# Optimization experiments

Measured on AMD Instinct MI355X. Metric: run time of the kernel, lower is better.

The kernel has to match this reference:

```python
import jax, jax.numpy as jnp
import numpy as np

N, E, DIM, H = 50000, 800000, 64, 2
HD = H * DIM


def setup_inputs() -> dict:
    key = jax.random.key(0)
    ks = jax.random.split(key, 16)
    s = 0.05
    return {
        "x": jax.random.normal(ks[0], (N, DIM), jnp.float32),
        "edge_index": jax.random.randint(ks[1], (2, E), 0, N, jnp.int64),
        "Wq": jax.random.normal(ks[2], (DIM, HD), jnp.float32) * s,
        "bq": jax.random.normal(ks[3], (HD,), jnp.float32) * s,
        "Wk": jax.random.normal(ks[4], (DIM, HD), jnp.float32) * s,
        "bk": jax.random.normal(ks[5], (HD,), jnp.float32) * s,
        "Wv": jax.random.normal(ks[6], (DIM, HD), jnp.float32) * s,
        "bv": jax.random.normal(ks[7], (HD,), jnp.float32) * s,
        "Wskip": jax.random.normal(ks[8], (DIM, HD), jnp.float32) * s,
        "bskip": jax.random.normal(ks[9], (HD,), jnp.float32) * s,
        "Wc": jax.random.normal(ks[10], (HD, DIM), jnp.float32) * s,
        "bc": jax.random.normal(ks[11], (DIM,), jnp.float32) * s,
        "gamma": jnp.ones((DIM,), jnp.float32),
        "beta": jnp.zeros((DIM,), jnp.float32),
    }


def reference(x, edge_index, Wq, bq, Wk, bk, Wv, bv, Wskip, bskip, Wc, bc, gamma, beta):
    src, dst = edge_index[0], edge_index[1]  # messages flow src -> dst
    # TransformerConv: per-head q/k/v projections, [N, H, D]
    q = (x @ Wq + bq).reshape(N, H, DIM)
    k = (x @ Wk + bk).reshape(N, H, DIM)
    v = (x @ Wv + bv).reshape(N, H, DIM)
    scale = 1.0 / np.sqrt(DIM).astype(np.float32)
    # edge-wise attention logits: [E, H]
    alpha = jnp.einsum('ehd,ehd->eh', q[dst], k[src]) * scale
    # segment softmax over incoming edges of each dst node (PyG softmax)
    amax = jax.ops.segment_max(alpha, dst, num_segments=N)
    a = jnp.exp(alpha - amax[dst])
    asum = jax.ops.segment_sum(a, dst, num_segments=N)
    a = a / (asum[dst] + 1e-16)
    # weighted scatter-aggregate of values: [N, H, D] -> concat heads
    out = jax.ops.segment_sum(a[:, :, None] * v[src], dst, num_segments=N)
    out = out.reshape(N, HD)
    # root/skip connection (root_weight=True default)
    out = out + (x @ Wskip + bskip)
    # concat linear: H*D -> dim
    out = out @ Wc + bc
    # pyg.LayerNorm default mode='graph': normalize over ALL nodes+features
    out = out - out.mean()
    out = out / (out.std() + 1e-5)  # std with unbiased=False (jnp default ddof=0)
    return out * gamma + beta
```

## Files before the change

### kernel.cpp

```cpp
#include <hip/hip_runtime.h>
#include <hip/hip_bf16.h>

#define N_NODES 50000
#define N_EDGES 800000
#define DIM 64
#define NHEAD 2
#define HD 128
#define NCOL 448
#define MAXDEG 64

#define ACH 2048
#define EDGE_BLKS 391

#define PREP_B 112
#define PROJ_B 782

#define QSCALE 0.18033688011112042f

typedef short bf16x8 __attribute__((ext_vector_type(8)));
typedef float f32x16 __attribute__((ext_vector_type(16)));
typedef float f32x2 __attribute__((ext_vector_type(2)));

__device__ __forceinline__ unsigned short f2bf(float f) {
    unsigned u = __float_as_uint(f);
    unsigned r = (u + 0x7fffu + ((u >> 16) & 1u)) >> 16;
    return (unsigned short)r;
}
__device__ __forceinline__ unsigned char f2fp8(float f) {
    int r = __builtin_amdgcn_cvt_pk_fp8_f32(f, f, 0, false);
    return (unsigned char)(r & 0xff);
}

__global__ __launch_bounds__(256) void k_pb(
    const int* __restrict__ ei,
    const float* __restrict__ Wq, const float* __restrict__ bq,
    const float* __restrict__ Wk, const float* __restrict__ bk,
    const float* __restrict__ Wv, const float* __restrict__ bv,
    const float* __restrict__ Wskip, const float* __restrict__ bskip,
    const float* __restrict__ Wc, const float* __restrict__ bc,
    unsigned short* __restrict__ WallT, float* __restrict__ ball,
    int* __restrict__ deg, unsigned short* __restrict__ elist,
    double* __restrict__ stats)
{
    const int t = threadIdx.x;
    if (blockIdx.x < PREP_B) {
        int gid = blockIdx.x * 256 + t;
        if (gid == 0) { stats[0] = 0.0; stats[1] = 0.0; }
        const int j = gid >> 6;
        const int d = gid & 63;
        float w, bb;
        if (j < 128) {
            w = Wq[d * HD + j] * QSCALE;
            bb = bq[j] * QSCALE;
        } else if (j < 256) {
            int jj = j - 128;
            w = Wk[d * HD + jj];
            bb = bk[jj];
        } else if (j < 384) {
            int jj = j - 256;
            int h = jj >> 6, jc = jj & 63;
            float s = 0.f, sb = 0.f;
            for (int c = 0; c < 64; c++) {
                float wc = Wc[(h * 64 + c) * DIM + jc];
                s  += Wv[d * HD + h * 64 + c] * wc;
                sb += bv[h * 64 + c] * wc;
            }
            w = s; bb = sb;
        } else {
            int jj = j - 384;
            float s = 0.f, sb = bc[jj];
            for (int c = 0; c < HD; c++) {
                float wc = Wc[c * DIM + jj];
                s  += Wskip[d * HD + c] * wc;
                sb += bskip[c] * wc;
            }
            w = s; bb = sb;
        }
        WallT[gid] = f2bf(w);
        if (d == 0) ball[j] = bb;
        return;
    }
    const int e0 = (blockIdx.x - PREP_B) * ACH;
#pragma unroll 2
    for (int i = t; i < ACH; i += 256) {
        int e = e0 + i;
        if (e < N_EDGES) {
            int src = ei[e];
            int d = ei[N_EDGES + e];
            int sl = atomicAdd(&deg[d], 1);
            if (sl < MAXDEG)
                elist[(size_t)d * MAXDEG + sl] = (unsigned short)src;
        }
    }
}

__global__ __launch_bounds__(256) void k_ep(
    const float* __restrict__ x,
    const unsigned short* __restrict__ WallT, const float* __restrict__ ball,
    float* __restrict__ q, unsigned char* __restrict__ kv, float* __restrict__ skipc)
{
    const int blk = blockIdx.x;
    const int t = threadIdx.x;
    const int w = t >> 6;
    const int lane = t & 63;
    const int col = lane & 31;
    const int khalf = lane >> 5;
    const int n0 = blk * 64 + (w >> 1) * 32;
    const int ct0 = (w & 1) * 7;
    const int rowbase = 4 * khalf;

    int nread = n0 + col; if (nread >= N_NODES) nread = N_NODES - 1;
    const float* ap = x + (size_t)nread * 64 + khalf * 8;
    bf16x8 afrag[4];
#pragma unroll
    for (int kk = 0; kk < 4; kk++) {
        float4 xa = *((const float4*)(ap + kk * 16));
        float4 xb4 = *((const float4*)(ap + kk * 16 + 4));
        bf16x8 f;
        f[0] = (short)f2bf(xa.x); f[1] = (short)f2bf(xa.y);
        f[2] = (short)f2bf(xa.z); f[3] = (short)f2bf(xa.w);
        f[4] = (short)f2bf(xb4.x); f[5] = (short)f2bf(xb4.y);
        f[6] = (short)f2bf(xb4.z); f[7] = (short)f2bf(xb4.w);
        afrag[kk] = f;
    }

    for (int tt = 0; tt < 7; tt++) {
        const int gc = (ct0 + tt) * 32 + col;
        const float b = ball[gc];
        f32x16 acc;
#pragma unroll
        for (int r = 0; r < 16; r++) acc[r] = b;
        const unsigned short* bp = WallT + (size_t)gc * 64 + khalf * 8;
#pragma unroll
        for (int kk = 0; kk < 4; kk++) {
            bf16x8 bfrag = *((const bf16x8*)(bp + kk * 16));
            acc = __builtin_amdgcn_mfma_f32_32x32x16_bf16(afrag[kk], bfrag, acc, 0, 0, 0);
        }
        if (gc < 128) {
#pragma unroll
            for (int r = 0; r < 16; r++) {
                int node = n0 + (r & 3) + 8 * (r >> 2) + rowbase;
                if (node < N_NODES) q[(size_t)node * HD + gc] = acc[r];
            }
        } else if (gc < 384) {
            int ch = gc - 128;
            int half = ch >> 7;
            int cc = ch & 127;
            int h = cc >> 6, c = cc & 63;
            int pos = half * 128 + ((c >> 3) << 4) + (h << 3) + (c & 7);
#pragma unroll
            for (int r = 0; r < 16; r++) {
                int node = n0 + (r & 3) + 8 * (r >> 2) + rowbase;
                if (node < N_NODES) kv[(size_t)node * 256 + pos] = f2fp8(acc[r]);
            }
        } else {
#pragma unroll
            for (int r = 0; r < 16; r++) {
                int node = n0 + (r & 3) + 8 * (r >> 2) + rowbase;
                if (node < N_NODES) skipc[(size_t)node * DIM + (gc - 384)] = acc[r];
            }
        }
    }
}

__global__ __launch_bounds__(256) void k_attn(
    const float* __restrict__ q, const unsigned char* __restrict__ kv,
    const float* __restrict__ skipc,
    const int* __restrict__ deg, const unsigned short* __restrict__ elist,
    float* __restrict__ out, float* __restrict__ parts)
{
    const int w = threadIdx.x >> 6;
    const int lane = threadIdx.x & 63;
    const int g = lane >> 3;
    const int j = lane & 7;
    const int n = blockIdx.x * 4 + w;
    const f32x2* qp = (const f32x2*)(q + (size_t)n * HD);
    f32x2 q0[4], q1[4];
#pragma unroll
    for (int i = 0; i < 4; i++) { q0[i] = qp[4 * j + i]; q1[i] = qp[32 + 4 * j + i]; }
    const int myE = elist[(size_t)n * MAXDEG + lane];
    f32x2 acc0[4], acc1[4];
#pragma unroll
    for (int i = 0; i < 4; i++) {
        acc0[i] = (f32x2){0.f, 0.f};
        acc1[i] = (f32x2){0.f, 0.f};
    }
    float l0 = 0.f, l1 = 0.f;
    int dg = deg[n]; if (dg > MAXDEG) dg = MAXDEG;
    for (int b0 = 0; b0 < dg; b0 += 8) {
        int idx = b0 + g;
        bool valid = idx < dg;
        int s = __shfl(myE, valid ? idx : 0, 64);
        const uint4* kp = (const uint4*)(kv + (size_t)s * 256);
        uint4 K = kp[j];
        uint4 V = kp[8 + j];
        f32x2 p0v = q0[0] * __builtin_amdgcn_cvt_pk_f32_fp8(K.x, false);
        p0v += q0[1] * __builtin_amdgcn_cvt_pk_f32_fp8(K.x, true);
        p0v += q0[2] * __builtin_amdgcn_cvt_pk_f32_fp8(K.y, false);
        p0v += q0[3] * __builtin_amdgcn_cvt_pk_f32_fp8(K.y, true);
        f32x2 p1v = q1[0] * __builtin_amdgcn_cvt_pk_f32_fp8(K.z, false);
        p1v += q1[1] * __builtin_amdgcn_cvt_pk_f32_fp8(K.z, true);
        p1v += q1[2] * __builtin_amdgcn_cvt_pk_f32_fp8(K.w, false);
        p1v += q1[3] * __builtin_amdgcn_cvt_pk_f32_fp8(K.w, true);
        float p0 = p0v[0] + p0v[1];
        float p1 = p1v[0] + p1v[1];
#pragma unroll
        for (int off = 1; off < 8; off <<= 1) {
            p0 += __shfl_xor(p0, off, 64);
            p1 += __shfl_xor(p1, off, 64);
        }
        float w0 = valid ? __builtin_amdgcn_exp2f(p0) : 0.f;
        float w1 = valid ? __builtin_amdgcn_exp2f(p1) : 0.f;
        l0 += w0; l1 += w1;
        f32x2 w0v = {w0, w0}, w1v = {w1, w1};
        acc0[0] += w0v * __builtin_amdgcn_cvt_pk_f32_fp8(V.x, false);
        acc0[1] += w0v * __builtin_amdgcn_cvt_pk_f32_fp8(V.x, true);
        acc0[2] += w0v * __builtin_amdgcn_cvt_pk_f32_fp8(V.y, false);
        acc0[3] += w0v * __builtin_amdgcn_cvt_pk_f32_fp8(V.y, true);
        acc1[0] += w1v * __builtin_amdgcn_cvt_pk_f32_fp8(V.z, false);
        acc1[1] += w1v * __builtin_amdgcn_cvt_pk_f32_fp8(V.z, true);
        acc1[2] += w1v * __builtin_amdgcn_cvt_pk_f32_fp8(V.w, false);
        acc1[3] += w1v * __builtin_amdgcn_cvt_pk_f32_fp8(V.w, true);
    }
    float* a0 = (float*)acc0;
    float* a1 = (float*)acc1;
#pragma unroll
    for (int off = 8; off < 64; off <<= 1) {
        l0 += __shfl_xor(l0, off, 64);
        l1 += __shfl_xor(l1, off, 64);
#pragma unroll
        for (int i = 0; i < 8; i++) {
            a0[i] += __shfl_xor(a0[i], off, 64);
            a1[i] += __shfl_xor(a1[i], off, 64);
        }
    }
    if (g == 0) {
        float inv0 = 1.f / (l0 + 1e-16f), inv1 = 1.f / (l1 + 1e-16f);
        const float4* sk = (const float4*)(skipc + (size_t)n * DIM);
        float4 sa = sk[2 * j], sb = sk[2 * j + 1];
        float o[8];
        o[0] = a0[0] * inv0 + a1[0] * inv1 + sa.x;
        o[1] = a0[1] * inv0 + a1[1] * inv1 + sa.y;
        o[2] = a0[2] * inv0 + a1[2] * inv1 + sa.z;
        o[3] = a0[3] * inv0 + a1[3] * inv1 + sa.w;
        o[4] = a0[4] * inv0 + a1[4] * inv1 + sb.x;
        o[5] = a0[5] * inv0 + a1[5] * inv1 + sb.y;
        o[6] = a0[6] * inv0 + a1[6] * inv1 + sb.z;
        o[7] = a0[7] * inv0 + a1[7] * inv1 + sb.w;
        float4 r0 = {o[0], o[1], o[2], o[3]}, r1 = {o[4], o[5], o[6], o[7]};
        float4* op = (float4*)(out + (size_t)n * DIM);
        op[2 * j] = r0; op[2 * j + 1] = r1;
        float s_ = 0.f, ss = 0.f;
#pragma unroll
        for (int i = 0; i < 8; i++) { s_ += o[i]; ss += o[i] * o[i]; }
#pragma unroll
        for (int off = 1; off < 8; off <<= 1) {
            s_ += __shfl_xor(s_, off, 64);
            ss += __shfl_xor(ss, off, 64);
        }
        if (j == 0) { parts[n] = s_; parts[N_NODES + n] = ss; }
    }
}

#define RED_BLOCKS 100
__global__ __launch_bounds__(256) void k_reduce(
    const float* __restrict__ parts, double* __restrict__ stats)
{
    double s = 0.0, ss = 0.0;
    for (int i = blockIdx.x * 256 + threadIdx.x; i < N_NODES; i += RED_BLOCKS * 256) {
        s  += (double)parts[i];
        ss += (double)parts[N_NODES + i];
    }
#pragma unroll
    for (int off = 32; off > 0; off >>= 1) {
        s  += __shfl_down(s, off);
        ss += __shfl_down(ss, off);
    }
    __shared__ double sdd[8];
    int wave = threadIdx.x >> 6;
    if ((threadIdx.x & 63) == 0) { sdd[wave * 2] = s; sdd[wave * 2 + 1] = ss; }
    __syncthreads();
    if (threadIdx.x == 0) {
        double S = 0.0, SS = 0.0;
        for (int w = 0; w < 4; w++) { S += sdd[w * 2]; SS += sdd[w * 2 + 1]; }
        atomicAdd(&stats[0], S);
        atomicAdd(&stats[1], SS);
    }
}

__global__ __launch_bounds__(256) void k_norm(
    float* __restrict__ out, const double* __restrict__ stats,
    const float* __restrict__ gamma, const float* __restrict__ beta)
{
    int i = blockIdx.x * 256 + threadIdx.x;
    if (i >= N_NODES * DIM / 4) return;
    const double cnt = (double)N_NODES * (double)DIM;
    double mean = stats[0] / cnt;
    double var  = stats[1] / cnt - mean * mean;
    if (var < 0.0) var = 0.0;
    float mf = (float)mean;
    float inv = 1.0f / ((float)sqrt(var) + 1e-5f);
    float4 v = ((const float4*)out)[i];
    float4 gv = ((const float4*)gamma)[i & 15];
    float4 bv2 = ((const float4*)beta)[i & 15];
    v.x = (v.x - mf) * inv * gv.x + bv2.x;
    v.y = (v.y - mf) * inv * gv.y + bv2.y;
    v.z = (v.z - mf) * inv * gv.z + bv2.z;
    v.w = (v.w - mf) * inv * gv.w + bv2.w;
    ((float4*)out)[i] = v;
}

extern "C" void kernel_launch(void* const* d_in, const int* in_sizes, int n_in,
                              void* d_out, int out_size, void* d_ws, size_t ws_size,
                              hipStream_t stream) {
    const float* x     = (const float*)d_in[0];
    const int*   ei    = (const int*)d_in[1];
    const float* Wq    = (const float*)d_in[2];
    const float* bq    = (const float*)d_in[3];
    const float* Wk    = (const float*)d_in[4];
    const float* bk    = (const float*)d_in[5];
    const float* Wv    = (const float*)d_in[6];
    const float* bv    = (const float*)d_in[7];
    const float* Wsk   = (const float*)d_in[8];
    const float* bsk   = (const float*)d_in[9];
    const float* Wc    = (const float*)d_in[10];
    const float* bc    = (const float*)d_in[11];
    const float* gamma = (const float*)d_in[12];
    const float* beta  = (const float*)d_in[13];
    float* out = (float*)d_out;

    float* ws = (float*)d_ws;
    const size_t NF = (size_t)N_NODES * HD;
    float* q = ws;
    unsigned char* kv = (unsigned char*)(ws + NF);
    float* skipc = (float*)(kv + (size_t)N_NODES * 256);
    unsigned short* WallT = (unsigned short*)(skipc + (size_t)N_NODES * DIM);
    float* ball   = (float*)(WallT + NCOL * 64);
    int* deg      = (int*)(ball + NCOL);
    unsigned short* elist = (unsigned short*)(deg + N_NODES);
    float* parts  = (float*)(elist + (size_t)N_NODES * MAXDEG);
    double* stats = (double*)(parts + (size_t)N_NODES * 2);

    hipMemsetAsync(deg, 0, N_NODES * sizeof(int), stream);
    hipLaunchKernelGGL(k_pb, dim3(PREP_B + EDGE_BLKS), dim3(256), 0, stream,
                       ei, Wq, bq, Wk, bk, Wv, bv, Wsk, bsk, Wc, bc,
                       WallT, ball, deg, elist, stats);
    hipLaunchKernelGGL(k_ep, dim3(PROJ_B), dim3(256), 0, stream,
                       x, WallT, ball, q, kv, skipc);
    hipLaunchKernelGGL(k_attn, dim3(N_NODES / 4), dim3(256), 0, stream,
                       q, kv, skipc, deg, elist, out, parts);
    hipLaunchKernelGGL(k_reduce, dim3(RED_BLOCKS), dim3(256), 0, stream, parts, stats);
    hipLaunchKernelGGL(k_norm, dim3(N_NODES * DIM / 4 / 256 + 1), dim3(256), 0, stream,
                       out, stats, gamma, beta);
}
```

Baseline: 210.3 us.

## Bin edges by destination block, build adjacency in LDS, fold stats reduction

Replaces per-edge global atomics on the degree array with a two-pass binning scheme. Edges are bucketed by destination>>8 using shared-memory histograms and are then turned into per-node adjacency lists with LDS atomics inside extra blocks of the projection kernel. It also drops the separate reduce kernel: attention accumulates stats with double atomics into 256 slots, and each norm block re-reduces those slots. This trades global atomic contention for an extra bins buffer pass, and adds a capacity cap per bin (BCAP) that could drop edges if a bin overflows.

Result: faster. 185.7 us (-11.7%).

```diff
diff --git a/kernel.cpp b/kernel.cpp
--- a/kernel.cpp
+++ b/kernel.cpp
@@ -9,8 +9,10 @@
 #define NCOL 448
 #define MAXDEG 64
 
+#define NBIN 196
+#define BCAP 6144
 #define ACH 2048
-#define EDGE_BLKS 391
+#define BIN_BLKS 391
 
 #define PREP_B 112
 #define PROJ_B 782
@@ -39,13 +41,13 @@
     const float* __restrict__ Wskip, const float* __restrict__ bskip,
     const float* __restrict__ Wc, const float* __restrict__ bc,
     unsigned short* __restrict__ WallT, float* __restrict__ ball,
-    int* __restrict__ deg, unsigned short* __restrict__ elist,
-    double* __restrict__ stats)
+    int* __restrict__ bincnt, unsigned* __restrict__ bins,
+    double* __restrict__ sacc)
 {
     const int t = threadIdx.x;
     if (blockIdx.x < PREP_B) {
+        if (blockIdx.x == 0) { sacc[t] = 0.0; sacc[256 + t] = 0.0; }
         int gid = blockIdx.x * 256 + t;
-        if (gid == 0) { stats[0] = 0.0; stats[1] = 0.0; }
         const int j = gid >> 6;
         const int d = gid & 63;
         float w, bb;
@@ -80,16 +82,39 @@
         if (d == 0) ball[j] = bb;
         return;
     }
+    __shared__ int hist[256];
+    __shared__ int gbase[256];
     const int e0 = (blockIdx.x - PREP_B) * ACH;
-#pragma unroll 2
-    for (int i = t; i < ACH; i += 256) {
-        int e = e0 + i;
+    hist[t] = 0;
+    __syncthreads();
+    unsigned pk8[8];
+    int bin8[8], sl8[8];
+#pragma unroll
+    for (int k = 0; k < 8; k++) {
+        int e = e0 + t + k * 256;
         if (e < N_EDGES) {
             int src = ei[e];
             int d = ei[N_EDGES + e];
-            int sl = atomicAdd(&deg[d], 1);
-            if (sl < MAXDEG)
-                elist[(size_t)d * MAXDEG + sl] = (unsigned short)src;
+            int bin = d >> 8;
+            pk8[k] = (unsigned)(((d & 255) << 16) | src);
+            bin8[k] = bin;
+            sl8[k] = atomicAdd(&hist[bin], 1);
+        } else {
+            bin8[k] = -1;
+        }
+    }
+    __syncthreads();
+    if (t < NBIN) {
+        int h = hist[t];
+        if (h > 0) gbase[t] = atomicAdd(&bincnt[t], h);
+    }
+    __syncthreads();
+#pragma unroll
+    for (int k = 0; k < 8; k++) {
+        int bin = bin8[k];
+        if (bin >= 0) {
+            int pos = gbase[bin] + sl8[k];
+            if (pos < BCAP) bins[(size_t)bin * BCAP + pos] = pk8[k];
         }
     }
 }
@@ -97,10 +122,35 @@
 __global__ __launch_bounds__(256) void k_ep(
     const float* __restrict__ x,
     const unsigned short* __restrict__ WallT, const float* __restrict__ ball,
-    float* __restrict__ q, unsigned char* __restrict__ kv, float* __restrict__ skipc)
+    float* __restrict__ q, unsigned char* __restrict__ kv, float* __restrict__ skipc,
+    const int* __restrict__ bincnt, const unsigned* __restrict__ bins,
+    int* __restrict__ deg, unsigned short* __restrict__ elist)
 {
     const int blk = blockIdx.x;
     const int t = threadIdx.x;
+    if (blk >= PROJ_B) {
+        const int bin = blk - PROJ_B;
+        __shared__ int nodecnt[256];
+        nodecnt[t] = 0;
+        __syncthreads();
+        int cnt = bincnt[bin]; if (cnt > BCAP) cnt = BCAP;
+        const unsigned* bp = bins + (size_t)bin * BCAP;
+        for (int i = t; i < cnt; i += 256) {
+            unsigned p = bp[i];
+            int local = p >> 16;
+            int src = p & 0xffff;
+            int sl = atomicAdd(&nodecnt[local], 1);
+            if (sl < MAXDEG)
+                elist[((size_t)((bin << 8) | local)) * MAXDEG + sl] = (unsigned short)src;
+        }
+        __syncthreads();
+        int node = (bin << 8) + t;
+        if (node < N_NODES) {
+            int dgv = nodecnt[t];
+            deg[node] = dgv > MAXDEG ? MAXDEG : dgv;
+        }
+        return;
+    }
     const int w = t >> 6;
     const int lane = t & 63;
     const int col = lane & 31;
@@ -167,7 +217,7 @@
     const float* __restrict__ q, const unsigned char* __restrict__ kv,
     const float* __restrict__ skipc,
     const int* __restrict__ deg, const unsigned short* __restrict__ elist,
-    float* __restrict__ out, float* __restrict__ parts)
+    float* __restrict__ out, double* __restrict__ sacc)
 {
     const int w = threadIdx.x >> 6;
     const int lane = threadIdx.x & 63;
@@ -258,48 +308,40 @@
             s_ += __shfl_xor(s_, off, 64);
             ss += __shfl_xor(ss, off, 64);
         }
-        if (j == 0) { parts[n] = s_; parts[N_NODES + n] = ss; }
-    }
-}
-
-#define RED_BLOCKS 100
-__global__ __launch_bounds__(256) void k_reduce(
-    const float* __restrict__ parts, double* __restrict__ stats)
+        if (j == 0) {
+            int slot = n & 255;
+            atomicAdd(&sacc[slot], (double)s_);
+            atomicAdd(&sacc[256 + slot], (double)ss);
+        }
+    }
+}
+
+__global__ __launch_bounds__(256) void k_norm(
+    float* __restrict__ out, const double* __restrict__ sacc,
+    const float* __restrict__ gamma, const float* __restrict__ beta)
 {
-    double s = 0.0, ss = 0.0;
-    for (int i = blockIdx.x * 256 + threadIdx.x; i < N_NODES; i += RED_BLOCKS * 256) {
-        s  += (double)parts[i];
-        ss += (double)parts[N_NODES + i];
-    }
+    const int t = threadIdx.x;
+    __shared__ double red[8];
+    double s = sacc[t];
+    double ss = sacc[256 + t];
 #pragma unroll
     for (int off = 32; off > 0; off >>= 1) {
         s  += __shfl_down(s, off);
         ss += __shfl_down(ss, off);
     }
-    __shared__ double sdd[8];
-    int wave = threadIdx.x >> 6;
-    if ((threadIdx.x & 63) == 0) { sdd[wave * 2] = s; sdd[wave * 2 + 1] = ss; }
+    int wv = t >> 6;
+    if ((t & 63) == 0) { red[wv * 2] = s; red[wv * 2 + 1] = ss; }
     __syncthreads();
-    if (threadIdx.x == 0) {
-        double S = 0.0, SS = 0.0;
-        for (int w = 0; w < 4; w++) { S += sdd[w * 2]; SS += sdd[w * 2 + 1]; }
-        atomicAdd(&stats[0], S);
-        atomicAdd(&stats[1], SS);
-    }
-}
-
-__global__ __launch_bounds__(256) void k_norm(
-    float* __restrict__ out, const double* __restrict__ stats,
-    const float* __restrict__ gamma, const float* __restrict__ beta)
-{
-    int i = blockIdx.x * 256 + threadIdx.x;
-    if (i >= N_NODES * DIM / 4) return;
+    double S  = red[0] + red[2] + red[4] + red[6];
+    double SS = red[1] + red[3] + red[5] + red[7];
     const double cnt = (double)N_NODES * (double)DIM;
-    double mean = stats[0] / cnt;
-    double var  = stats[1] / cnt - mean * mean;
+    double mean = S / cnt;
+    double var  = SS / cnt - mean * mean;
     if (var < 0.0) var = 0.0;
     float mf = (float)mean;
     float inv = 1.0f / ((float)sqrt(var) + 1e-5f);
+    int i = blockIdx.x * 256 + t;
+    if (i >= N_NODES * DIM / 4) return;
     float4 v = ((const float4*)out)[i];
     float4 gv = ((const float4*)gamma)[i & 15];
     float4 bv2 = ((const float4*)beta)[i & 15];
@@ -329,27 +371,27 @@
     const float* beta  = (const float*)d_in[13];
     float* out = (float*)d_out;
 
-    float* ws = (float*)d_ws;
+    double* sacc = (double*)d_ws;
+    float* ws = (float*)(sacc + 512);
     const size_t NF = (size_t)N_NODES * HD;
     float* q = ws;
     unsigned char* kv = (unsigned char*)(ws + NF);
     float* skipc = (float*)(kv + (size_t)N_NODES * 256);
     unsigned short* WallT = (unsigned short*)(skipc + (size_t)N_NODES * DIM);
     float* ball   = (float*)(WallT + NCOL * 64);
-    int* deg      = (int*)(ball + NCOL);
+    int* bincnt   = (int*)(ball + NCOL);
+    unsigned* bins = (unsigned*)(bincnt + 256);
+    int* deg      = (int*)(bins + (size_t)NBIN * BCAP);
     unsigned short* elist = (unsigned short*)(deg + N_NODES);
-    float* parts  = (float*)(elist + (size_t)N_NODES * MAXDEG);
-    double* stats = (double*)(parts + (size_t)N_NODES * 2);
-
-    hipMemsetAsync(deg, 0, N_NODES * sizeof(int), stream);
-    hipLaunchKernelGGL(k_pb, dim3(PREP_B + EDGE_BLKS), dim3(256), 0, stream,
+
+    hipMemsetAsync(bincnt, 0, 256 * sizeof(int), stream);
+    hipLaunchKernelGGL(k_pb, dim3(PREP_B + BIN_BLKS), dim3(256), 0, stream,
                        ei, Wq, bq, Wk, bk, Wv, bv, Wsk, bsk, Wc, bc,
-                       WallT, ball, deg, elist, stats);
-    hipLaunchKernelGGL(k_ep, dim3(PROJ_B), dim3(256), 0, stream,
-                       x, WallT, ball, q, kv, skipc);
+                       WallT, ball, bincnt, bins, sacc);
+    hipLaunchKernelGGL(k_ep, dim3(PROJ_B + NBIN), dim3(256), 0, stream,
+                       x, WallT, ball, q, kv, skipc, bincnt, bins, deg, elist);
     hipLaunchKernelGGL(k_attn, dim3(N_NODES / 4), dim3(256), 0, stream,
-                       q, kv, skipc, deg, elist, out, parts);
-    hipLaunchKernelGGL(k_reduce, dim3(RED_BLOCKS), dim3(256), 0, stream, parts, stats);
+                       q, kv, skipc, deg, elist, out, sacc);
     hipLaunchKernelGGL(k_norm, dim3(N_NODES * DIM / 4 / 256 + 1), dim3(256), 0, stream,
-                       out, stats, gamma, beta);
-}
+                       out, sacc, gamma, beta);
+}
```
